# Optimization experiments

Measured on AMD Instinct MI355X. Metric: run time of the kernel, lower is better.

## Reference

```python
import jax, jax.numpy as jnp
import numpy as np

NEG_SLOPE = 0.01  # F.leaky_relu default
NUM_GRAPHS = 64


def sage_conv(x, src, dst, W_l, b_l, W_r):
    """PyG SAGEConv (mean aggr): lin_l(mean_j x_j) + lin_r(x_i)."""
    n = x.shape[0]
    msg = x[src]                                               # [E, C] gather
    agg = jax.ops.segment_sum(msg, dst, num_segments=n)        # [N, C] scatter-add
    deg = jax.ops.segment_sum(jnp.ones_like(dst, dtype=x.dtype), dst, num_segments=n)
    mean = agg / jnp.maximum(deg, 1.0)[:, None]
    return mean @ W_l + b_l + x @ W_r


def setup_inputs() -> dict:
    key = jax.random.key(0)
    ks = jax.random.split(key, 12)
    N, E, C, H, O = 50000, 600000, 128, 128, 2
    x = jax.random.normal(ks[0], (N, C), dtype=jnp.float32)
    edge_index = jax.random.randint(ks[1], (2, E), 0, N, dtype=jnp.int64)
    batch = jnp.sort(jax.random.randint(ks[2], (N,), 0, NUM_GRAPHS, dtype=jnp.int64))

    def lin(k, fin, fout):
        return jax.random.normal(k, (fin, fout), dtype=jnp.float32) / np.sqrt(fin)

    return {
        "x": x, "edge_index": edge_index, "batch": batch,
        "W1_l": lin(ks[3], C, H), "b1": jnp.zeros((H,), jnp.float32), "W1_r": lin(ks[4], C, H),
        "W2_l": lin(ks[5], H, H), "b2": jnp.zeros((H,), jnp.float32), "W2_r": lin(ks[6], H, H),
        "W3_l": lin(ks[7], H, H), "b3": jnp.zeros((H,), jnp.float32), "W3_r": lin(ks[8], H, H),
        "W_fc": lin(ks[9], H, O), "b_fc": jnp.zeros((O,), jnp.float32),
    }


def reference(x, edge_index, batch, W1_l, b1, W1_r, W2_l, b2, W2_r,
              W3_l, b3, W3_r, W_fc, b_fc):
    src, dst = edge_index[0], edge_index[1]
    h = jax.nn.leaky_relu(sage_conv(x, src, dst, W1_l, b1, W1_r), NEG_SLOPE)
    h = jax.nn.leaky_relu(sage_conv(h, src, dst, W2_l, b2, W2_r), NEG_SLOPE)
    h = jax.nn.leaky_relu(sage_conv(h, src, dst, W3_l, b3, W3_r), NEG_SLOPE)
    pooled = jax.ops.segment_max(h, batch, num_segments=NUM_GRAPHS)  # global_max_pool
    return pooled @ W_fc + b_fc
```

## Files before the change

### kernel.cpp

```cpp
#include <hip/hip_runtime.h>
#include <hip/hip_bf16.h>

#define NEG_SLOPE 0.01f
#define C 128
#define NGRAPH 64

typedef short short8 __attribute__((ext_vector_type(8)));
typedef float f32x4 __attribute__((ext_vector_type(4)));
typedef unsigned short ushort;

__device__ __forceinline__ unsigned fmap(float x){
  unsigned b = __float_as_uint(x);
  return (b & 0x80000000u) ? ~b : (b | 0x80000000u);
}
__device__ __forceinline__ float funmap(unsigned k){
  return (k & 0x80000000u) ? __uint_as_float(k & 0x7FFFFFFFu) : __uint_as_float(~k);
}

__device__ __forceinline__ ushort bf16_rne(float a){
  unsigned u = __float_as_uint(a);
  return (ushort)((u + 0x7FFFu + ((u >> 16) & 1u)) >> 16);
}
__device__ __forceinline__ float b2f(ushort h){
  return __uint_as_float(((unsigned)h) << 16);
}

__device__ __forceinline__ void lds_dma16(const void* g, void* l){
  __builtin_amdgcn_global_load_lds(
      (const __attribute__((address_space(1))) unsigned int*)(void*)g,
      (__attribute__((address_space(3))) unsigned int*)(void*)l, 16, 0, 0);
}

__global__ void to_bf16(const float* __restrict__ in, ushort* __restrict__ o, int n){
  int i = (blockIdx.x * blockDim.x + threadIdx.x) * 4;
  if(i >= n) return;
  float4 v = *(const float4*)(in + i);
  ushort4 r = make_ushort4(bf16_rne(v.x), bf16_rne(v.y), bf16_rne(v.z), bf16_rne(v.w));
  *(ushort4*)(o + i) = r;
}

__global__ void deg_kernel(const int* __restrict__ dst, int* __restrict__ deg, int E){
  int e = blockIdx.x * blockDim.x + threadIdx.x;
  if(e < E) atomicAdd(&deg[dst[e]], 1);
}

__global__ void scan_block(const int* __restrict__ deg, int* __restrict__ incl,
                           int* __restrict__ bsum, int N){
  __shared__ int sm[1024];
  int t = threadIdx.x;
  int i = blockIdx.x * 1024 + t;
  int v = (i < N) ? deg[i] : 0;
  sm[t] = v;
  __syncthreads();
  for(int off = 1; off < 1024; off <<= 1){
    int a = (t >= off) ? sm[t - off] : 0;
    __syncthreads();
    sm[t] += a;
    __syncthreads();
  }
  if(i < N) incl[i] = sm[t];
  if(t == 1023) bsum[blockIdx.x] = sm[t];
}

__global__ void scan_bsum(const int* __restrict__ bsum, int* __restrict__ boff, int nb){
  __shared__ int sm[64];
  int t = threadIdx.x;
  sm[t] = (t < nb) ? bsum[t] : 0;
  __syncthreads();
  for(int off = 1; off < 64; off <<= 1){
    int a = (t >= off) ? sm[t - off] : 0;
    __syncthreads();
    sm[t] += a;
    __syncthreads();
  }
  if(t < nb) boff[t] = sm[t] - bsum[t];
}

__global__ void finalize_rows(const int* __restrict__ incl, const int* __restrict__ deg,
                              const int* __restrict__ boff, int* __restrict__ rows,
                              float* __restrict__ inv_deg, int N, int E){
  int i = blockIdx.x * blockDim.x + threadIdx.x;
  if(i < N){
    rows[i] = incl[i] - deg[i] + boff[i >> 10];
    inv_deg[i] = 1.0f / fmaxf((float)deg[i], 1.0f);
  }
  if(i == 0) rows[N] = E;
}

__global__ void csr_fill_kernel(const int* __restrict__ src, const int* __restrict__ dst,
                                const int* __restrict__ row_start, int* __restrict__ cursor,
                                int* __restrict__ csr, int E){
  int e = blockIdx.x * blockDim.x + threadIdx.x;
  if(e >= E) return;
  int d = dst[e];
  int p = atomicAdd(&cursor[d], 1);
  csr[row_start[d] + p] = src[e];
}

__global__ __launch_bounds__(256) void agg_csr_g16(
    const ushort* __restrict__ xb, const int* __restrict__ csr,
    const int* __restrict__ row_start, const float* __restrict__ inv_deg,
    ushort* __restrict__ mb, int N)
{
  int tid = threadIdx.x;
  int node = blockIdx.x * 16 + (tid >> 4);
  if(node >= N) return;
  int g15 = tid & 15;
  int gbase = tid & 48;
  int beg = row_start[node], end = row_start[node + 1];
  float a[8] = {0.f, 0.f, 0.f, 0.f, 0.f, 0.f, 0.f, 0.f};

  for(int base = beg; base < end; base += 16){
    int cnt = end - base; if(cnt > 16) cnt = 16;
    int s_l = (base + g15 < end) ? csr[base + g15] : 0;
    int j = 0;
    for(; j + 4 <= cnt; j += 4){
      int s0 = __shfl(s_l, gbase + j + 0, 64);
      int s1 = __shfl(s_l, gbase + j + 1, 64);
      int s2 = __shfl(s_l, gbase + j + 2, 64);
      int s3 = __shfl(s_l, gbase + j + 3, 64);
      short8 v0 = *(const short8*)(xb + (long long)s0 * C + g15 * 8);
      short8 v1 = *(const short8*)(xb + (long long)s1 * C + g15 * 8);
      short8 v2 = *(const short8*)(xb + (long long)s2 * C + g15 * 8);
      short8 v3 = *(const short8*)(xb + (long long)s3 * C + g15 * 8);
#pragma unroll
      for(int k = 0; k < 8; k++){
        a[k] += b2f((ushort)v0[k]);
        a[k] += b2f((ushort)v1[k]);
        a[k] += b2f((ushort)v2[k]);
        a[k] += b2f((ushort)v3[k]);
      }
    }
    for(; j < cnt; j++){
      int s = __shfl(s_l, gbase + j, 64);
      short8 v = *(const short8*)(xb + (long long)s * C + g15 * 8);
#pragma unroll
      for(int k = 0; k < 8; k++) a[k] += b2f((ushort)v[k]);
    }
  }
  float sc = inv_deg[node];
  short8 o;
#pragma unroll
  for(int k = 0; k < 8; k++) o[k] = (short)bf16_rne(a[k] * sc);
  *(short8*)(mb + (long long)node * C + g15 * 8) = o;
}

__global__ void pack_kernel(const float* __restrict__ Wl, const float* __restrict__ Wr,
                            short* __restrict__ Bpk){
  int idx = blockIdx.x * blockDim.x + threadIdx.x;
  if(idx >= 2 * C * C) return;
  int k = idx >> 7, n = idx & 127;
  float w = (k < C) ? Wl[k * C + n] : Wr[(k - C) * C + n];
  ushort hi = bf16_rne(w);
  float r = w - b2f(hi);
  ushort lo = bf16_rne(r);
  int kstep = k >> 5, kg = (k >> 3) & 3, j = k & 7;
  int pos = ((kstep * 4 + kg) * C + n) * 8 + j;
  Bpk[pos] = (short)hi;
  Bpk[pos + 32768] = (short)lo;
}

__global__ __launch_bounds__(256, 2) void gemm_mfma5(
    const ushort* __restrict__ Amean, const ushort* __restrict__ Ax,
    const short* __restrict__ Bpk, const float* __restrict__ bias,
    ushort* __restrict__ Hout, int M,
    const int* __restrict__ batch, unsigned* __restrict__ pooled)
{
  __shared__ __align__(16) ushort As[64 * 32];
  int tid = threadIdx.x;
  int bm = blockIdx.x * 64;
  int lane = tid & 63;
  int wn = tid >> 6;
  int lg = lane >> 4;
  int lm = lane & 15;

  int srow = tid >> 2;
  int sslice = (tid & 3) ^ ((tid >> 3) & 3);
  int grow = bm + srow; if(grow >= M) grow = M - 1;
  const long long goff = (long long)grow * C + sslice * 8;
  ushort* ldsbase = As + wn * 512;

  f32x4 acc[4][2];
#pragma unroll
  for(int i = 0; i < 4; i++)
#pragma unroll
    for(int j = 0; j < 2; j++)
      acc[i][j] = (f32x4){0.f, 0.f, 0.f, 0.f};

  short8 bh[2][2], bl[2][2];
  auto loadB = [&](int ks, int buf){
#pragma unroll
    for(int j = 0; j < 2; j++){
      const short* bp = Bpk + (((ks * 4 + lg) * C) + wn * 32 + j * 16 + lm) * 8;
      bh[buf][j] = *(const short8*)bp;
      bl[buf][j] = *(const short8*)(bp + 32768);
    }
  };

  loadB(0, 0);
#pragma unroll
  for(int ks = 0; ks < 8; ks++){
    if(ks > 0) __syncthreads();
    const ushort* Ap = (ks < 4) ? Amean : Ax;
    lds_dma16(Ap + goff + (ks & 3) * 32, ldsbase);
    if(ks < 7) loadB(ks + 1, (ks + 1) & 1);
    __syncthreads();

    short8 af[4];
#pragma unroll
    for(int i = 0; i < 4; i++){
      int r = i * 16 + lm;
      int slot = lg ^ ((r >> 1) & 3);
      af[i] = *(const short8*)(As + r * 32 + slot * 8);
    }
    int b = ks & 1;
#pragma unroll
    for(int i = 0; i < 4; i++)
#pragma unroll
      for(int j = 0; j < 2; j++){
        acc[i][j] = __builtin_amdgcn_mfma_f32_16x16x32_bf16(af[i], bh[b][j], acc[i][j], 0, 0, 0);
        acc[i][j] = __builtin_amdgcn_mfma_f32_16x16x32_bf16(af[i], bl[b][j], acc[i][j], 0, 0, 0);
      }
  }

  if(pooled == nullptr){
#pragma unroll
    for(int j = 0; j < 2; j++){
      int col = wn * 32 + j * 16 + lm;
      float bv = bias[col];
#pragma unroll
      for(int i = 0; i < 4; i++){
#pragma unroll
        for(int reg = 0; reg < 4; reg++){
          int row = bm + i * 16 + lg * 4 + reg;
          if(row < M){
            float v = acc[i][j][reg] + bv;
            v = v > 0.f ? v : NEG_SLOPE * v;
            Hout[(long long)row * C + col] = bf16_rne(v);
          }
        }
      }
    }
  }else{
#pragma unroll
    for(int i = 0; i < 4; i++){
      int row0 = bm + i * 16 + lg * 4;
      if(row0 >= M) continue;
      bool whole = (row0 + 3 < M);
      int g0 = batch[row0];
      bool same = whole && (batch[row0 + 3] == g0);
#pragma unroll
      for(int j = 0; j < 2; j++){
        int col = wn * 32 + j * 16 + lm;
        float bv = bias[col];
        float v0 = acc[i][j][0] + bv; v0 = v0 > 0.f ? v0 : NEG_SLOPE * v0;
        float v1 = acc[i][j][1] + bv; v1 = v1 > 0.f ? v1 : NEG_SLOPE * v1;
        float v2 = acc[i][j][2] + bv; v2 = v2 > 0.f ? v2 : NEG_SLOPE * v2;
        float v3 = acc[i][j][3] + bv; v3 = v3 > 0.f ? v3 : NEG_SLOPE * v3;
        if(same){
          float m01 = fmaxf(v0, v1), m23 = fmaxf(v2, v3);
          atomicMax(&pooled[g0 * C + col], fmap(fmaxf(m01, m23)));
        }else{
          float vv[4] = {v0, v1, v2, v3};
#pragma unroll
          for(int reg = 0; reg < 4; reg++){
            int row = row0 + reg;
            if(row < M) atomicMax(&pooled[batch[row] * C + col], fmap(vv[reg]));
          }
        }
      }
    }
  }
}

__global__ void fc_kernel(const unsigned* __restrict__ pooled_u, const float* __restrict__ Wfc,
                          const float* __restrict__ bfc, float* __restrict__ out){
  int t = threadIdx.x;
  int g = t >> 1, o = t & 1;
  float s = bfc[o];
  for(int k = 0; k < C; k++)
    s += funmap(pooled_u[g * C + k]) * Wfc[k * 2 + o];
  out[g * 2 + o] = s;
}

extern "C" void kernel_launch(void* const* d_in, const int* in_sizes, int n_in,
                              void* d_out, int out_size, void* d_ws, size_t ws_size,
                              hipStream_t stream) {
  const float* x    = (const float*)d_in[0];
  const int*   ei   = (const int*)d_in[1];
  const int*   batch= (const int*)d_in[2];
  const float* W1l  = (const float*)d_in[3];
  const float* b1   = (const float*)d_in[4];
  const float* W1r  = (const float*)d_in[5];
  const float* W2l  = (const float*)d_in[6];
  const float* b2   = (const float*)d_in[7];
  const float* W2r  = (const float*)d_in[8];
  const float* W3l  = (const float*)d_in[9];
  const float* b3   = (const float*)d_in[10];
  const float* W3r  = (const float*)d_in[11];
  const float* Wfc  = (const float*)d_in[12];
  const float* bfc  = (const float*)d_in[13];
  float* out = (float*)d_out;

  const int N = in_sizes[0] / C;
  const int E = in_sizes[1] / 2;
  const int* srcv = ei;
  const int* dstv = ei + E;

  char* ws = (char*)d_ws;
  size_t off = 0;
  auto alloc = [&](size_t bytes) -> void* {
    void* p = ws + off;
    off += (bytes + 255) & ~(size_t)255;
    return p;
  };
  int*      deg    = (int*)alloc((size_t)N * 4);
  float*    inv_d  = (float*)alloc((size_t)N * 4);
  int*      incl   = (int*)alloc((size_t)N * 4);
  int*      bsum   = (int*)alloc((size_t)64 * 4);
  int*      boff   = (int*)alloc((size_t)64 * 4);
  int*      rows   = (int*)alloc((size_t)(N + 1) * 4);
  int*      cursor = (int*)alloc((size_t)N * 4);
  int*      csr    = (int*)alloc((size_t)E * 4);
  ushort*   xb     = (ushort*)alloc((size_t)N * C * 2);
  ushort*   mb     = (ushort*)alloc((size_t)N * C * 2);
  ushort*   h1b    = (ushort*)alloc((size_t)N * C * 2);
  short*    B1     = (short*)alloc((size_t)2 * 2 * C * C * 2);
  short*    B2     = (short*)alloc((size_t)2 * 2 * C * C * 2);
  short*    B3     = (short*)alloc((size_t)2 * 2 * C * C * 2);
  unsigned* pooled = (unsigned*)alloc((size_t)NGRAPH * C * 4);

  hipMemsetAsync(deg, 0, (size_t)N * 4, stream);
  hipMemsetAsync(cursor, 0, (size_t)N * 4, stream);
  hipMemsetAsync(pooled, 0, (size_t)NGRAPH * C * 4, stream);

  const int nb = (N + 1023) / 1024;
  to_bf16<<<(N * C / 4 + 255) / 256, 256, 0, stream>>>(x, xb, N * C);
  deg_kernel<<<(E + 255) / 256, 256, 0, stream>>>(dstv, deg, E);
  scan_block<<<nb, 1024, 0, stream>>>(deg, incl, bsum, N);
  scan_bsum<<<1, 64, 0, stream>>>(bsum, boff, nb);
  finalize_rows<<<(N + 255) / 256, 256, 0, stream>>>(incl, deg, boff, rows, inv_d, N, E);
  csr_fill_kernel<<<(E + 255) / 256, 256, 0, stream>>>(srcv, dstv, rows, cursor, csr, E);

  pack_kernel<<<(2 * C * C + 255) / 256, 256, 0, stream>>>(W1l, W1r, B1);
  pack_kernel<<<(2 * C * C + 255) / 256, 256, 0, stream>>>(W2l, W2r, B2);
  pack_kernel<<<(2 * C * C + 255) / 256, 256, 0, stream>>>(W3l, W3r, B3);

  int gemmblocks = (N + 63) / 64;
  int aggblocks = (N + 15) / 16;

  agg_csr_g16<<<aggblocks, 256, 0, stream>>>(xb, csr, rows, inv_d, mb, N);
  gemm_mfma5<<<gemmblocks, 256, 0, stream>>>(mb, xb, B1, b1, h1b, N, nullptr, nullptr);
  agg_csr_g16<<<aggblocks, 256, 0, stream>>>(h1b, csr, rows, inv_d, mb, N);
  gemm_mfma5<<<gemmblocks, 256, 0, stream>>>(mb, h1b, B2, b2, xb, N, nullptr, nullptr);
  agg_csr_g16<<<aggblocks, 256, 0, stream>>>(xb, csr, rows, inv_d, mb, N);
  gemm_mfma5<<<gemmblocks, 256, 0, stream>>>(mb, xb, B3, b3, nullptr, N, batch, pooled);

  fc_kernel<<<1, 128, 0, stream>>>(pooled, Wfc, bfc, out);
}
```

Measured before the change: 312.4 us.

## Fuse neighbor aggregation into GEMM per layer and merge prep kernels

Each SAGE layer now runs as one kernel: every 64-row block first gathers and averages its nodes' neighbor features into an LDS tile, then runs the MFMA GEMM reading the mean half from LDS and the self half via DMA. This drops the intermediate mean buffer write and read plus three kernel launches. The bf16 conversion, degree count and weight packing are merged into one multi-role prep kernel, and the three memsets become one by placing the zeroed buffers next to each other. The trade-off is that the gather phase and the GEMM phase no longer overlap across different kernels, and the larger LDS footprint may lower occupancy.

Result: faster. 287.2 us (-8.1%).

```diff
diff --git a/kernel.cpp b/kernel.cpp
--- a/kernel.cpp
+++ b/kernel.cpp
@@ -31,17 +31,45 @@
       (__attribute__((address_space(3))) unsigned int*)(void*)l, 16, 0, 0);
 }
 
-__global__ void to_bf16(const float* __restrict__ in, ushort* __restrict__ o, int n){
-  int i = (blockIdx.x * blockDim.x + threadIdx.x) * 4;
-  if(i >= n) return;
-  float4 v = *(const float4*)(in + i);
-  ushort4 r = make_ushort4(bf16_rne(v.x), bf16_rne(v.y), bf16_rne(v.z), bf16_rne(v.w));
-  *(ushort4*)(o + i) = r;
-}
-
-__global__ void deg_kernel(const int* __restrict__ dst, int* __restrict__ deg, int E){
-  int e = blockIdx.x * blockDim.x + threadIdx.x;
-  if(e < E) atomicAdd(&deg[dst[e]], 1);
+__global__ void prep_kernel(const float* __restrict__ x, ushort* __restrict__ xb, int nx4,
+                            const int* __restrict__ dst, int* __restrict__ deg, int E,
+                            const float* __restrict__ W1l, const float* __restrict__ W1r,
+                            const float* __restrict__ W2l, const float* __restrict__ W2r,
+                            const float* __restrict__ W3l, const float* __restrict__ W3r,
+                            short* __restrict__ B1, short* __restrict__ B2,
+                            short* __restrict__ B3,
+                            int nblk_x, int nblk_deg){
+  int bid = blockIdx.x;
+  if(bid < nblk_x){
+    int i = (bid * 256 + threadIdx.x) * 4;
+    if(i < nx4){
+      float4 v = *(const float4*)(x + i);
+      ushort4 r = make_ushort4(bf16_rne(v.x), bf16_rne(v.y), bf16_rne(v.z), bf16_rne(v.w));
+      *(ushort4*)(xb + i) = r;
+    }
+    return;
+  }
+  bid -= nblk_x;
+  if(bid < nblk_deg){
+    int e = bid * 256 + threadIdx.x;
+    if(e < E) atomicAdd(&deg[dst[e]], 1);
+    return;
+  }
+  bid -= nblk_deg;
+  int set = bid >> 7;
+  int idx = (bid & 127) * 256 + threadIdx.x;
+  const float* Wl = (set == 0) ? W1l : (set == 1) ? W2l : W3l;
+  const float* Wr = (set == 0) ? W1r : (set == 1) ? W2r : W3r;
+  short* Bpk      = (set == 0) ? B1  : (set == 1) ? B2  : B3;
+  int k = idx >> 7, n = idx & 127;
+  float w = (k < C) ? Wl[k * C + n] : Wr[(k - C) * C + n];
+  ushort hi = bf16_rne(w);
+  float r = w - b2f(hi);
+  ushort lo = bf16_rne(r);
+  int kstep = k >> 5, kg = (k >> 3) & 3, j = k & 7;
+  int pos = ((kstep * 4 + kg) * C + n) * 8 + j;
+  Bpk[pos] = (short)hi;
+  Bpk[pos + 32768] = (short)lo;
 }
 
 __global__ void scan_block(const int* __restrict__ deg, int* __restrict__ incl,
@@ -97,76 +125,15 @@
   csr[row_start[d] + p] = src[e];
 }
 
-__global__ __launch_bounds__(256) void agg_csr_g16(
-    const ushort* __restrict__ xb, const int* __restrict__ csr,
-    const int* __restrict__ row_start, const float* __restrict__ inv_deg,
-    ushort* __restrict__ mb, int N)
-{
-  int tid = threadIdx.x;
-  int node = blockIdx.x * 16 + (tid >> 4);
-  if(node >= N) return;
-  int g15 = tid & 15;
-  int gbase = tid & 48;
-  int beg = row_start[node], end = row_start[node + 1];
-  float a[8] = {0.f, 0.f, 0.f, 0.f, 0.f, 0.f, 0.f, 0.f};
-
-  for(int base = beg; base < end; base += 16){
-    int cnt = end - base; if(cnt > 16) cnt = 16;
-    int s_l = (base + g15 < end) ? csr[base + g15] : 0;
-    int j = 0;
-    for(; j + 4 <= cnt; j += 4){
-      int s0 = __shfl(s_l, gbase + j + 0, 64);
-      int s1 = __shfl(s_l, gbase + j + 1, 64);
-      int s2 = __shfl(s_l, gbase + j + 2, 64);
-      int s3 = __shfl(s_l, gbase + j + 3, 64);
-      short8 v0 = *(const short8*)(xb + (long long)s0 * C + g15 * 8);
-      short8 v1 = *(const short8*)(xb + (long long)s1 * C + g15 * 8);
-      short8 v2 = *(const short8*)(xb + (long long)s2 * C + g15 * 8);
-      short8 v3 = *(const short8*)(xb + (long long)s3 * C + g15 * 8);
-#pragma unroll
-      for(int k = 0; k < 8; k++){
-        a[k] += b2f((ushort)v0[k]);
-        a[k] += b2f((ushort)v1[k]);
-        a[k] += b2f((ushort)v2[k]);
-        a[k] += b2f((ushort)v3[k]);
-      }
-    }
-    for(; j < cnt; j++){
-      int s = __shfl(s_l, gbase + j, 64);
-      short8 v = *(const short8*)(xb + (long long)s * C + g15 * 8);
-#pragma unroll
-      for(int k = 0; k < 8; k++) a[k] += b2f((ushort)v[k]);
-    }
-  }
-  float sc = inv_deg[node];
-  short8 o;
-#pragma unroll
-  for(int k = 0; k < 8; k++) o[k] = (short)bf16_rne(a[k] * sc);
-  *(short8*)(mb + (long long)node * C + g15 * 8) = o;
-}
-
-__global__ void pack_kernel(const float* __restrict__ Wl, const float* __restrict__ Wr,
-                            short* __restrict__ Bpk){
-  int idx = blockIdx.x * blockDim.x + threadIdx.x;
-  if(idx >= 2 * C * C) return;
-  int k = idx >> 7, n = idx & 127;
-  float w = (k < C) ? Wl[k * C + n] : Wr[(k - C) * C + n];
-  ushort hi = bf16_rne(w);
-  float r = w - b2f(hi);
-  ushort lo = bf16_rne(r);
-  int kstep = k >> 5, kg = (k >> 3) & 3, j = k & 7;
-  int pos = ((kstep * 4 + kg) * C + n) * 8 + j;
-  Bpk[pos] = (short)hi;
-  Bpk[pos + 32768] = (short)lo;
-}
-
-__global__ __launch_bounds__(256, 2) void gemm_mfma5(
-    const ushort* __restrict__ Amean, const ushort* __restrict__ Ax,
+__global__ __launch_bounds__(256, 2) void layer_fused(
+    const ushort* __restrict__ xin, const int* __restrict__ csr,
+    const int* __restrict__ rowp, const float* __restrict__ inv_deg,
     const short* __restrict__ Bpk, const float* __restrict__ bias,
     ushort* __restrict__ Hout, int M,
     const int* __restrict__ batch, unsigned* __restrict__ pooled)
 {
-  __shared__ __align__(16) ushort As[64 * 32];
+  __shared__ ushort Ms[64 * 136];
+  __shared__ __align__(16) ushort Xs[64 * 32];
   int tid = threadIdx.x;
   int bm = blockIdx.x * 64;
   int lane = tid & 63;
@@ -174,11 +141,55 @@
   int lg = lane >> 4;
   int lm = lane & 15;
 
+  {
+    int grp = tid >> 4, g15 = tid & 15, gbase = tid & 48;
+    for(int nn = grp; nn < 64; nn += 16){
+      int node = bm + nn;
+      float a[8] = {0.f, 0.f, 0.f, 0.f, 0.f, 0.f, 0.f, 0.f};
+      if(node < M){
+        int beg = rowp[node], end = rowp[node + 1];
+        for(int base = beg; base < end; base += 16){
+          int cnt = end - base; if(cnt > 16) cnt = 16;
+          int s_l = (base + g15 < end) ? csr[base + g15] : 0;
+          int j = 0;
+          for(; j + 4 <= cnt; j += 4){
+            int s0 = __shfl(s_l, gbase + j + 0, 64);
+            int s1 = __shfl(s_l, gbase + j + 1, 64);
+            int s2 = __shfl(s_l, gbase + j + 2, 64);
+            int s3 = __shfl(s_l, gbase + j + 3, 64);
+            short8 v0 = *(const short8*)(xin + (long long)s0 * C + g15 * 8);
+            short8 v1 = *(const short8*)(xin + (long long)s1 * C + g15 * 8);
+            short8 v2 = *(const short8*)(xin + (long long)s2 * C + g15 * 8);
+            short8 v3 = *(const short8*)(xin + (long long)s3 * C + g15 * 8);
+#pragma unroll
+            for(int k = 0; k < 8; k++){
+              a[k] += b2f((ushort)v0[k]); a[k] += b2f((ushort)v1[k]);
+              a[k] += b2f((ushort)v2[k]); a[k] += b2f((ushort)v3[k]);
+            }
+          }
+          for(; j < cnt; j++){
+            int s = __shfl(s_l, gbase + j, 64);
+            short8 v = *(const short8*)(xin + (long long)s * C + g15 * 8);
+#pragma unroll
+            for(int k = 0; k < 8; k++) a[k] += b2f((ushort)v[k]);
+          }
+        }
+        float sc = inv_deg[node];
+#pragma unroll
+        for(int k = 0; k < 8; k++) a[k] *= sc;
+      }
+      short8 o;
+#pragma unroll
+      for(int k = 0; k < 8; k++) o[k] = (short)bf16_rne(a[k]);
+      *(short8*)(Ms + nn * 136 + g15 * 8) = o;
+    }
+  }
+
   int srow = tid >> 2;
   int sslice = (tid & 3) ^ ((tid >> 3) & 3);
   int grow = bm + srow; if(grow >= M) grow = M - 1;
   const long long goff = (long long)grow * C + sslice * 8;
-  ushort* ldsbase = As + wn * 512;
+  ushort* ldsbase = Xs + wn * 512;
 
   f32x4 acc[4][2];
 #pragma unroll
@@ -196,22 +207,30 @@
       bl[buf][j] = *(const short8*)(bp + 32768);
     }
   };
-
   loadB(0, 0);
+  __syncthreads();
+
 #pragma unroll
   for(int ks = 0; ks < 8; ks++){
-    if(ks > 0) __syncthreads();
-    const ushort* Ap = (ks < 4) ? Amean : Ax;
-    lds_dma16(Ap + goff + (ks & 3) * 32, ldsbase);
+    if(ks >= 4){
+      if(ks > 4) __syncthreads();
+      lds_dma16(xin + goff + (ks - 4) * 32, ldsbase);
+    }
     if(ks < 7) loadB(ks + 1, (ks + 1) & 1);
-    __syncthreads();
+    if(ks >= 4) __syncthreads();
 
     short8 af[4];
-#pragma unroll
-    for(int i = 0; i < 4; i++){
-      int r = i * 16 + lm;
-      int slot = lg ^ ((r >> 1) & 3);
-      af[i] = *(const short8*)(As + r * 32 + slot * 8);
+    if(ks < 4){
+#pragma unroll
+      for(int i = 0; i < 4; i++)
+        af[i] = *(const short8*)(Ms + (i * 16 + lm) * 136 + ks * 32 + lg * 8);
+    }else{
+#pragma unroll
+      for(int i = 0; i < 4; i++){
+        int r = i * 16 + lm;
+        int slot = lg ^ ((r >> 1) & 3);
+        af[i] = *(const short8*)(Xs + r * 32 + slot * 8);
+      }
     }
     int b = ks & 1;
 #pragma unroll
@@ -315,46 +334,44 @@
     return p;
   };
   int*      deg    = (int*)alloc((size_t)N * 4);
+  int*      cursor = (int*)alloc((size_t)N * 4);
+  unsigned* pooled = (unsigned*)alloc((size_t)NGRAPH * C * 4);
+  size_t    zbytes = off;
   float*    inv_d  = (float*)alloc((size_t)N * 4);
   int*      incl   = (int*)alloc((size_t)N * 4);
   int*      bsum   = (int*)alloc((size_t)64 * 4);
   int*      boff   = (int*)alloc((size_t)64 * 4);
   int*      rows   = (int*)alloc((size_t)(N + 1) * 4);
-  int*      cursor = (int*)alloc((size_t)N * 4);
   int*      csr    = (int*)alloc((size_t)E * 4);
   ushort*   xb     = (ushort*)alloc((size_t)N * C * 2);
-  ushort*   mb     = (ushort*)alloc((size_t)N * C * 2);
   ushort*   h1b    = (ushort*)alloc((size_t)N * C * 2);
   short*    B1     = (short*)alloc((size_t)2 * 2 * C * C * 2);
   short*    B2     = (short*)alloc((size_t)2 * 2 * C * C * 2);
   short*    B3     = (short*)alloc((size_t)2 * 2 * C * C * 2);
-  unsigned* pooled = (unsigned*)alloc((size_t)NGRAPH * C * 4);
-
-  hipMemsetAsync(deg, 0, (size_t)N * 4, stream);
-  hipMemsetAsync(cursor, 0, (size_t)N * 4, stream);
-  hipMemsetAsync(pooled, 0, (size_t)NGRAPH * C * 4, stream);
+
+  hipMemsetAsync(deg, 0, zbytes, stream);
+
+  const int nbx  = (N * C / 4 + 255) / 256;
+  const int nbd  = (E + 255) / 256;
+  const int nbp  = 3 * 128;
+  prep_kernel<<<nbx + nbd + nbp, 256, 0, stream>>>(
+      x, xb, N * C, dstv, deg, E,
+      W1l, W1r, W2l, W2r, W3l, W3r, B1, B2, B3, nbx, nbd);
 
   const int nb = (N + 1023) / 1024;
-  to_bf16<<<(N * C / 4 + 255) / 256, 256, 0, stream>>>(x, xb, N * C);
-  deg_kernel<<<(E + 255) / 256, 256, 0, stream>>>(dstv, deg, E);
   scan_block<<<nb, 1024, 0, stream>>>(deg, incl, bsum, N);
   scan_bsum<<<1, 64, 0, stream>>>(bsum, boff, nb);
   finalize_rows<<<(N + 255) / 256, 256, 0, stream>>>(incl, deg, boff, rows, inv_d, N, E);
   csr_fill_kernel<<<(E + 255) / 256, 256, 0, stream>>>(srcv, dstv, rows, cursor, csr, E);
 
-  pack_kernel<<<(2 * C * C + 255) / 256, 256, 0, stream>>>(W1l, W1r, B1);
-  pack_kernel<<<(2 * C * C + 255) / 256, 256, 0, stream>>>(W2l, W2r, B2);
-  pack_kernel<<<(2 * C * C + 255) / 256, 256, 0, stream>>>(W3l, W3r, B3);
-
-  int gemmblocks = (N + 63) / 64;
-  int aggblocks = (N + 15) / 16;
-
-  agg_csr_g16<<<aggblocks, 256, 0, stream>>>(xb, csr, rows, inv_d, mb, N);
-  gemm_mfma5<<<gemmblocks, 256, 0, stream>>>(mb, xb, B1, b1, h1b, N, nullptr, nullptr);
-  agg_csr_g16<<<aggblocks, 256, 0, stream>>>(h1b, csr, rows, inv_d, mb, N);
-  gemm_mfma5<<<gemmblocks, 256, 0, stream>>>(mb, h1b, B2, b2, xb, N, nullptr, nullptr);
-  agg_csr_g16<<<aggblocks, 256, 0, stream>>>(xb, csr, rows, inv_d, mb, N);
-  gemm_mfma5<<<gemmblocks, 256, 0, stream>>>(mb, xb, B3, b3, nullptr, N, batch, pooled);
+  int lblocks = (N + 63) / 64;
+
+  layer_fused<<<lblocks, 256, 0, stream>>>(xb, csr, rows, inv_d, B1, b1,
+                                           h1b, N, nullptr, nullptr);
+  layer_fused<<<lblocks, 256, 0, stream>>>(h1b, csr, rows, inv_d, B2, b2,
+                                           xb, N, nullptr, nullptr);
+  layer_fused<<<lblocks, 256, 0, stream>>>(xb, csr, rows, inv_d, B3, b3,
+                                           nullptr, N, batch, pooled);
 
   fc_kernel<<<1, 128, 0, stream>>>(pooled, Wfc, bfc, out);
 }
```
